# Optimization experiments

Measured on AMD Instinct MI355X. Metric: run time of the kernel, lower is better.

Reference implementation:

```python
import jax, jax.numpy as jnp
import numpy as np

D_MODEL = 1024
NUM_HEADS = 16
SEG = 512            # segment_size
DIL = 4              # dilation_rate
HEAD_DIM = D_MODEL // NUM_HEADS


def setup_inputs() -> dict:
    key = jax.random.key(0)
    ks = jax.random.split(key, 5)
    B, S = 4, 4096
    sc = D_MODEL ** -0.5  # keep projected activations O(1) so softmax is not saturated
    def w(k):
        return jax.random.normal(k, (D_MODEL, D_MODEL), jnp.float32) * sc
    z = jnp.zeros((D_MODEL,), jnp.float32)
    return {
        "x": jax.random.normal(ks[0], (B, S, D_MODEL), jnp.float32),
        "Wq": w(ks[1]), "bq": z,
        "Wk": w(ks[2]), "bk": z,
        "Wv": w(ks[3]), "bv": z,
        "Wo": w(ks[4]), "bo": z,
    }


def reference(x, Wq, bq, Wk, bk, Wv, bv, Wo, bo):
    B, S, D = x.shape
    H, hd, seg, r = NUM_HEADS, HEAD_DIM, SEG, DIL
    scaling = hd ** -0.5

    Q = x @ Wq + bq
    K = x @ Wk + bk
    V = x @ Wv + bv

    pad = (-S) % seg
    if pad:
        Q = jnp.pad(Q, ((0, 0), (0, pad), (0, 0)))
        K = jnp.pad(K, ((0, 0), (0, pad), (0, 0)))
        V = jnp.pad(V, ((0, 0), (0, pad), (0, 0)))
    n = (S + pad) // seg          # num_segments
    sd = seg // r                 # dilated positions per segment per head

    # [B, n, sd, r, H, hd]: position within segment = t*r + offset
    def split(t):
        return t.reshape(B, n, sd, r, H, hd)

    offs = jnp.arange(H) % r      # per-head dilation offset sj = j % r
    hidx = jnp.arange(H)
    # vectorized per-head dilated gather -> [B, n, sd, H, hd]
    Qs = split(Q)[:, :, :, offs, hidx, :]
    Ks = split(K)[:, :, :, offs, hidx, :]
    Vs = split(V)[:, :, :, offs, hidx, :]

    # diagonal q.k score per dilated position, softmax over the segment's dilated positions
    scores = jnp.einsum('bnshd,bnshd->bnsh', Qs, Ks) * scaling
    probs = jax.nn.softmax(scores, axis=2)
    attn = probs[..., None] * Vs  # [B, n, sd, H, hd]

    # scatter back to each head's dilated positions; other positions stay zero
    out = jnp.zeros((B, n, sd, r, H, hd), x.dtype)
    out = out.at[:, :, :, offs, hidx, :].set(attn)
    out = out.reshape(B, n * seg, D)[:, :S]
    return out @ Wo + bo
```

## Files before the change

### kernel.cpp

```cpp
#include <hip/hip_runtime.h>
#include <hip/hip_bf16.h>

typedef unsigned short u16;
typedef unsigned int u32;
typedef __attribute__((ext_vector_type(8))) __bf16 bf16x8;
typedef __attribute__((ext_vector_type(4))) float f32x4;

#define NB 4
#define SQ 4096
#define DM 1024
#define RPC 4096

__device__ __forceinline__ u16 f2b(float f) {
  u32 u = __builtin_bit_cast(u32, f);
  u32 r = u + 0x7fffu + ((u >> 16) & 1u);
  return (u16)(r >> 16);
}
__device__ __forceinline__ u32 cvt2(float lo, float hi) {
  u16 a = __builtin_bit_cast(u16, __float2bfloat16(lo));
  u16 b = __builtin_bit_cast(u16, __float2bfloat16(hi));
  return (u32)a | ((u32)b << 16);
}
__device__ __forceinline__ float dot2(u32 q, u32 k) {
  float ql = __builtin_bit_cast(float, q << 16);
  float qh = __builtin_bit_cast(float, q & 0xffff0000u);
  float kl = __builtin_bit_cast(float, k << 16);
  float kh = __builtin_bit_cast(float, k & 0xffff0000u);
  return ql * kl + qh * kh;
}
__device__ __forceinline__ u32 mul2(u32 v, float p) {
  float lo = __builtin_bit_cast(float, v << 16) * p;
  float hi = __builtin_bit_cast(float, v & 0xffff0000u) * p;
  return (u32)f2b(lo) | ((u32)f2b(hi) << 16);
}
__device__ __forceinline__ void gll16(const void* g, void* l) {
  __builtin_amdgcn_global_load_lds(
      (const __attribute__((address_space(1))) void*)g,
      (__attribute__((address_space(3))) void*)l, 16, 0, 0);
}

__global__ __launch_bounds__(256) void trans_qkv(const float* __restrict__ Wq,
                                                 const float* __restrict__ Wk,
                                                 const float* __restrict__ Wv,
                                                 u16* __restrict__ WTp) {
  __shared__ float T[64][65];
  const int k0 = blockIdx.x * 64, j0 = blockIdx.y * 64, c = blockIdx.z;
  const int msel = j0 >> 8;
  const float* W = (msel == 0) ? Wq : ((msel == 1) ? Wk : Wv);
  const int slot = (j0 & 255) >> 6;
  const int colbase = (c + 4 * slot) * 64;
  const int tid = threadIdx.x;
  const int rr = tid >> 6, cc = tid & 63;
#pragma unroll
  for (int it = 0; it < 16; ++it) {
    const int kk = rr + it * 4;
    T[kk][cc] = W[(size_t)(k0 + kk) * 1024 + colbase + cc];
  }
  __syncthreads();
  const int k64 = k0 >> 6;
  const int u = cc >> 3, e = cc & 7;
#pragma unroll
  for (int it = 0; it < 16; ++it) {
    const int jj = rr + it * 4;
    const int j = j0 + jj;
    const int n0 = j >> 8, nrow = j & 255;
    const int p = u ^ (nrow & 7);
    WTp[((size_t)((c * 3 + n0) * 16 + k64)) * 16384 + nrow * 64 + p * 8 + e] = f2b(T[cc][jj]);
  }
}

__global__ __launch_bounds__(256) void trans_wo(const float* __restrict__ Wo,
                                                u16* __restrict__ WoTp) {
  __shared__ float T[64][65];
  const int j0 = blockIdx.x * 64, e0 = blockIdx.y * 64, c = blockIdx.z;
  const int rowbase = c * 64 + (j0 >> 6) * 256;
  const int tid = threadIdx.x;
  const int rr = tid >> 6, cc = tid & 63;
#pragma unroll
  for (int it = 0; it < 16; ++it) {
    const int jj = rr + it * 4;
    T[jj][cc] = Wo[(size_t)(rowbase + jj) * 1024 + e0 + cc];
  }
  __syncthreads();
  const int k64 = j0 >> 6;
  const int u = cc >> 3, e = cc & 7;
#pragma unroll
  for (int it = 0; it < 16; ++it) {
    const int ee = rr + it * 4;
    const int n = e0 + ee;
    const int n0 = n >> 7, nrow = n & 127;
    const int p = u ^ (nrow & 7);
    WoTp[((size_t)((c * 8 + n0) * 4 + k64)) * 8192 + nrow * 64 + p * 8 + e] = f2b(T[cc][ee]);
  }
}

__global__ __launch_bounds__(256) void bias_pack(const float* __restrict__ bq,
                                                 const float* __restrict__ bk,
                                                 const float* __restrict__ bv,
                                                 float* __restrict__ biasp) {
  const int idx = blockIdx.x * 256 + threadIdx.x;
  if (idx >= 3072) return;
  const int c = idx / 768, j = idx % 768;
  const int msel = j >> 8, jj = j & 255;
  const int col = (c + 4 * (jj >> 6)) * 64 + (jj & 63);
  const float* bb = (msel == 0) ? bq : ((msel == 1) ? bk : bv);
  biasp[idx] = bb[col];
}

__global__ __launch_bounds__(256, 2) void gemm_qkv(const float* __restrict__ x,
                                                   const u16* __restrict__ WTp,
                                                   const float* __restrict__ biasp,
                                                   u16* __restrict__ QKV) {
  __shared__ __align__(16) u16 As[8192];
  __shared__ __align__(16) u16 Bs[16384];
  const int c = blockIdx.z, m0 = blockIdx.y, n0 = blockIdx.x;
  const int tid = threadIdx.x;
  const int lane = tid & 63, w = tid >> 6;
  const int wm = w >> 1, wn = w & 1;
  const int l15 = lane & 15, l16 = lane >> 4;

  f32x4 acc[4][8];
#pragma unroll
  for (int i = 0; i < 4; ++i)
#pragma unroll
    for (int j = 0; j < 8; ++j) acc[i][j] = (f32x4){0.f, 0.f, 0.f, 0.f};

  const int rbase = m0 * 128;
  const int b = rbase >> 10;
  const int sbase = ((rbase & 1023) << 2) + c;
  const float* xA = x + (size_t)(b * SQ + sbase) * DM;

  const int arow = tid >> 3, au = tid & 7;
  int awoff[4];
#pragma unroll
  for (int w4 = 0; w4 < 4; ++w4) {
    const int row = w4 * 32 + arow;
    awoff[w4] = row * 64 + ((au ^ (row & 7)) << 3);
  }
  const u16* Bsrc = WTp + (size_t)((c * 3 + n0) * 16) * 16384 + tid * 8;
  char* BsW = (char*)Bs + w * 1024;

  int aoff[2][4], boff[2][8];
#pragma unroll
  for (int kk = 0; kk < 2; ++kk) {
    const int unit = kk * 4 + l16;
#pragma unroll
    for (int mf = 0; mf < 4; ++mf) {
      const int row = wm * 64 + mf * 16 + l15;
      aoff[kk][mf] = row * 64 + ((unit ^ (row & 7)) << 3);
    }
#pragma unroll
    for (int nf = 0; nf < 8; ++nf) {
      const int row = wn * 128 + nf * 16 + l15;
      boff[kk][nf] = row * 64 + ((unit ^ (row & 7)) << 3);
    }
  }

  float4 av[8];
#pragma unroll
  for (int w4 = 0; w4 < 4; ++w4) {
    const float* s = xA + (size_t)(w4 * 32 + arow) * (4 * DM) + au * 8;
    av[2 * w4] = *reinterpret_cast<const float4*>(s);
    av[2 * w4 + 1] = *reinterpret_cast<const float4*>(s + 4);
  }

#pragma unroll 1
  for (int k64 = 0; k64 < 16; ++k64) {
    __syncthreads();
#pragma unroll
    for (int it = 0; it < 8; ++it)
      gll16(Bsrc + (size_t)k64 * 16384 + it * 2048, BsW + it * 4096);
#pragma unroll
    for (int w4 = 0; w4 < 4; ++w4) {
      uint4 pk;
      pk.x = cvt2(av[2 * w4].x, av[2 * w4].y);
      pk.y = cvt2(av[2 * w4].z, av[2 * w4].w);
      pk.z = cvt2(av[2 * w4 + 1].x, av[2 * w4 + 1].y);
      pk.w = cvt2(av[2 * w4 + 1].z, av[2 * w4 + 1].w);
      *reinterpret_cast<uint4*>(&As[awoff[w4]]) = pk;
    }
    __syncthreads();
    if (k64 < 15) {
      const int k0 = (k64 + 1) * 64;
#pragma unroll
      for (int w4 = 0; w4 < 4; ++w4) {
        const float* s = xA + (size_t)(w4 * 32 + arow) * (4 * DM) + k0 + au * 8;
        av[2 * w4] = *reinterpret_cast<const float4*>(s);
        av[2 * w4 + 1] = *reinterpret_cast<const float4*>(s + 4);
      }
    }
#pragma unroll
    for (int kk = 0; kk < 2; ++kk) {
      bf16x8 af[4], bv[8];
#pragma unroll
      for (int mf = 0; mf < 4; ++mf) af[mf] = *reinterpret_cast<const bf16x8*>(&As[aoff[kk][mf]]);
#pragma unroll
      for (int nf = 0; nf < 8; ++nf) bv[nf] = *reinterpret_cast<const bf16x8*>(&Bs[boff[kk][nf]]);
#pragma unroll
      for (int mf = 0; mf < 4; ++mf)
#pragma unroll
        for (int nf = 0; nf < 8; ++nf)
          acc[mf][nf] = __builtin_amdgcn_mfma_f32_16x16x32_bf16(af[mf], bv[nf], acc[mf][nf], 0, 0, 0);
    }
  }

  u16* outc = QKV + (size_t)c * RPC * 768;
#pragma unroll
  for (int mf = 0; mf < 4; ++mf) {
#pragma unroll
    for (int nf = 0; nf < 8; ++nf) {
      const int gcol = n0 * 256 + wn * 128 + nf * 16 + l15;
      const float bias = biasp[c * 768 + gcol];
#pragma unroll
      for (int jj = 0; jj < 4; ++jj) {
        const int rowt = wm * 64 + mf * 16 + l16 * 4 + jj;
        outc[(size_t)(rbase + rowt) * 768 + gcol] = f2b(acc[mf][nf][jj] + bias);
      }
    }
  }
}

__global__ __launch_bounds__(256) void attn_k(const u16* __restrict__ QKV,
                                              u16* __restrict__ attnYp) {
  __shared__ float sc[4][128];
  const int blk = blockIdx.x;
  const int c = blk >> 5, b = (blk >> 3) & 3, n = blk & 7;
  const int r0 = b * 1024 + n * 128;
  const int m0 = b * 8 + n;
  const u16* base = QKV + ((size_t)c * RPC + r0) * 768;
  const int tid = threadIdx.x;
#pragma unroll
  for (int it = 0; it < 2; ++it) {
    const int tt = tid + it * 256;
    const int t = tt & 127, slot = tt >> 7;
    const u16* q = base + (size_t)t * 768 + slot * 64;
    float s = 0.f;
#pragma unroll
    for (int dd = 0; dd < 8; ++dd) {
      uint4 qa = *reinterpret_cast<const uint4*>(q + dd * 8);
      uint4 ka = *reinterpret_cast<const uint4*>(q + 256 + dd * 8);
      s += dot2(qa.x, ka.x) + dot2(qa.y, ka.y) + dot2(qa.z, ka.z) + dot2(qa.w, ka.w);
    }
    sc[slot][t] = s * 0.125f;
  }
  __syncthreads();
  const int w = tid >> 6, lane = tid & 63;
  float v0 = sc[w][lane], v1 = sc[w][lane + 64];
  float m = fmaxf(v0, v1);
#pragma unroll
  for (int off = 32; off; off >>= 1) m = fmaxf(m, __shfl_xor(m, off));
  float e0 = __expf(v0 - m), e1 = __expf(v1 - m);
  float ssum = e0 + e1;
#pragma unroll
  for (int off = 32; off; off >>= 1) ssum += __shfl_xor(ssum, off);
  const float inv = 1.f / ssum;
  sc[w][lane] = e0 * inv;
  sc[w][lane + 64] = e1 * inv;
  __syncthreads();
  u16* yout = attnYp + (size_t)((c * 32 + m0) * 4) * 8192;
#pragma unroll
  for (int it = 0; it < 16; ++it) {
    const int vi = tid + it * 256;
    const int t = vi >> 5, c8 = vi & 31;
    const float p = sc[c8 >> 3][t];
    uint4 va = *reinterpret_cast<const uint4*>(base + (size_t)t * 768 + 512 + c8 * 8);
    uint4 ra;
    ra.x = mul2(va.x, p); ra.y = mul2(va.y, p); ra.z = mul2(va.z, p); ra.w = mul2(va.w, p);
    const int k64 = c8 >> 3, uu = c8 & 7, pp = uu ^ (t & 7);
    *reinterpret_cast<uint4*>(yout + k64 * 8192 + t * 64 + pp * 8) = ra;
  }
}

__global__ __launch_bounds__(256) void gemm_out(const u16* __restrict__ attnYp,
                                                const u16* __restrict__ WoTp,
                                                const float* __restrict__ bo,
                                                float* __restrict__ out) {
  __shared__ __align__(16) u16 As[8192];
  __shared__ __align__(16) u16 Bs[8192];
  const int c = blockIdx.z, m0 = blockIdx.y, n0 = blockIdx.x;
  const int tid = threadIdx.x;
  const int lane = tid & 63, w = tid >> 6;
  const int wm = w >> 1, wn = w & 1;
  const int l15 = lane & 15, l16 = lane >> 4;

  f32x4 acc[4][4];
#pragma unroll
  for (int i = 0; i < 4; ++i)
#pragma unroll
    for (int j = 0; j < 4; ++j) acc[i][j] = (f32x4){0.f, 0.f, 0.f, 0.f};

  const u16* Asrc = attnYp + (size_t)((c * 32 + m0) * 4) * 8192 + tid * 8;
  const u16* Bsrc = WoTp + (size_t)((c * 8 + n0) * 4) * 8192 + tid * 8;
  char* AsW = (char*)As + w * 1024;
  char* BsW = (char*)Bs + w * 1024;

  int aoff[2][4], boff[2][4];
#pragma unroll
  for (int kk = 0; kk < 2; ++kk) {
    const int unit = kk * 4 + l16;
#pragma unroll
    for (int f = 0; f < 4; ++f) {
      const int ra = wm * 64 + f * 16 + l15;
      aoff[kk][f] = ra * 64 + ((unit ^ (ra & 7)) << 3);
      const int rb = wn * 64 + f * 16 + l15;
      boff[kk][f] = rb * 64 + ((unit ^ (rb & 7)) << 3);
    }
  }

#pragma unroll 1
  for (int k64 = 0; k64 < 4; ++k64) {
    __syncthreads();
#pragma unroll
    for (int it = 0; it < 4; ++it) {
      gll16(Asrc + (size_t)k64 * 8192 + it * 2048, AsW + it * 4096);
      gll16(Bsrc + (size_t)k64 * 8192 + it * 2048, BsW + it * 4096);
    }
    __syncthreads();
#pragma unroll
    for (int kk = 0; kk < 2; ++kk) {
      bf16x8 af[4], bfv[4];
#pragma unroll
      for (int f = 0; f < 4; ++f) {
        af[f] = *reinterpret_cast<const bf16x8*>(&As[aoff[kk][f]]);
        bfv[f] = *reinterpret_cast<const bf16x8*>(&Bs[boff[kk][f]]);
      }
#pragma unroll
      for (int mf = 0; mf < 4; ++mf)
#pragma unroll
        for (int nf = 0; nf < 4; ++nf)
          acc[mf][nf] = __builtin_amdgcn_mfma_f32_16x16x32_bf16(af[mf], bfv[nf], acc[mf][nf], 0, 0, 0);
    }
  }

  const int rbase = m0 * 128;
  const int b = rbase >> 10;
  const int sbase = ((rbase & 1023) << 2) + c;
  float* outp = out + (size_t)(b * SQ + sbase) * DM;
#pragma unroll
  for (int mf = 0; mf < 4; ++mf) {
#pragma unroll
    for (int nf = 0; nf < 4; ++nf) {
      const int gcol = n0 * 128 + wn * 64 + nf * 16 + l15;
      const float bias = bo[gcol];
#pragma unroll
      for (int jj = 0; jj < 4; ++jj) {
        const int rowt = wm * 64 + mf * 16 + l16 * 4 + jj;
        outp[(size_t)rowt * (4 * DM) + gcol] = acc[mf][nf][jj] + bias;
      }
    }
  }
}

extern "C" void kernel_launch(void* const* d_in, const int* in_sizes, int n_in,
                              void* d_out, int out_size, void* d_ws, size_t ws_size,
                              hipStream_t stream) {
  const float* x  = (const float*)d_in[0];
  const float* Wq = (const float*)d_in[1];
  const float* bq = (const float*)d_in[2];
  const float* Wk = (const float*)d_in[3];
  const float* bk = (const float*)d_in[4];
  const float* Wv = (const float*)d_in[5];
  const float* bv = (const float*)d_in[6];
  const float* Wo = (const float*)d_in[7];
  const float* bo = (const float*)d_in[8];
  float* out = (float*)d_out;

  char* ws = (char*)d_ws;
  u16*   WTp   = (u16*)(ws);
  float* biasp = (float*)(ws + 6291456);
  u16*   WoTp  = (u16*)(ws + 6303744);
  u16*   QKV   = (u16*)(ws + 8400896);
  u16*   attnYp= (u16*)(ws + 33566720);

  trans_qkv<<<dim3(16, 12, 4), 256, 0, stream>>>(Wq, Wk, Wv, WTp);
  bias_pack<<<12, 256, 0, stream>>>(bq, bk, bv, biasp);
  trans_wo<<<dim3(4, 16, 4), 256, 0, stream>>>(Wo, WoTp);
  gemm_qkv<<<dim3(3, 32, 4), 256, 0, stream>>>(x, WTp, biasp, QKV);
  attn_k<<<128, 256, 0, stream>>>(QKV, attnYp);
  gemm_out<<<dim3(8, 32, 4), 256, 0, stream>>>(attnYp, WoTp, bo, out);
}
```

Baseline: 99.21 us.

## Double-buffer both GEMMs with 512-thread 256-row tiles and swizzled block order

Both GEMMs move to 512-thread blocks with 256-row tiles and double-buffered LDS. Explicit vmcnt/lgkmcnt waits and raw barriers let the next K-tile load overlap the MFMAs on the current one, and setprio raises MFMA priority. Weight packing is re-laid for the new tile widths (192 and 256 columns), and the grid is linearised with a remapped block index to change L2 locality. Attention now uses 256 blocks, each handling half the V columns. The hand-written waitcnt counts are fragile: a wrong count would cause a race, and the larger LDS footprint may reduce occupancy.

```diff
diff --git a/kernel.cpp b/kernel.cpp
--- a/kernel.cpp
+++ b/kernel.cpp
@@ -10,6 +10,11 @@
 #define SQ 4096
 #define DM 1024
 #define RPC 4096
+#define S4 (4 * DM)
+
+#define VMCNT(n) asm volatile("s_waitcnt vmcnt(" #n ")" ::: "memory")
+#define LGKM0()  asm volatile("s_waitcnt lgkmcnt(0)" ::: "memory")
+#define BARRIER() asm volatile("s_barrier" ::: "memory")
 
 __device__ __forceinline__ u16 f2b(float f) {
   u32 u = __builtin_bit_cast(u32, f);
@@ -63,9 +68,9 @@
   for (int it = 0; it < 16; ++it) {
     const int jj = rr + it * 4;
     const int j = j0 + jj;
-    const int n0 = j >> 8, nrow = j & 255;
-    const int p = u ^ (nrow & 7);
-    WTp[((size_t)((c * 3 + n0) * 16 + k64)) * 16384 + nrow * 64 + p * 8 + e] = f2b(T[cc][jj]);
+    const int n0 = j / 192, nrow = j - n0 * 192;
+    WTp[((size_t)((c * 4 + n0) * 16 + k64)) * 12288 + nrow * 64 + (((u ^ (nrow & 7))) << 3) + e] =
+        f2b(T[cc][jj]);
   }
 }
 
@@ -88,9 +93,9 @@
   for (int it = 0; it < 16; ++it) {
     const int ee = rr + it * 4;
     const int n = e0 + ee;
-    const int n0 = n >> 7, nrow = n & 127;
-    const int p = u ^ (nrow & 7);
-    WoTp[((size_t)((c * 8 + n0) * 4 + k64)) * 8192 + nrow * 64 + p * 8 + e] = f2b(T[cc][ee]);
+    const int n0 = n >> 8, nrow = n & 255;
+    WoTp[((size_t)((c * 4 + n0) * 4 + k64)) * 16384 + nrow * 64 + (((u ^ (nrow & 7))) << 3) + e] =
+        f2b(T[cc][ee]);
   }
 }
 
@@ -107,109 +112,138 @@
   biasp[idx] = bb[col];
 }
 
-__global__ __launch_bounds__(256, 2) void gemm_qkv(const float* __restrict__ x,
+__global__ __launch_bounds__(512, 2) void gemm_qkv(const float* __restrict__ x,
                                                    const u16* __restrict__ WTp,
                                                    const float* __restrict__ biasp,
                                                    u16* __restrict__ QKV) {
-  __shared__ __align__(16) u16 As[8192];
-  __shared__ __align__(16) u16 Bs[16384];
-  const int c = blockIdx.z, m0 = blockIdx.y, n0 = blockIdx.x;
+  __shared__ __align__(16) u16 As[2][16384];
+  __shared__ __align__(16) u16 Bs[2][12288];
+  const int p = blockIdx.x;
+  const int L = (p & 7) * 32 + (p >> 3);
+  const int c = L >> 6, rem = L & 63;
+  const int m0 = rem >> 2, n0 = rem & 3;
   const int tid = threadIdx.x;
   const int lane = tid & 63, w = tid >> 6;
   const int wm = w >> 1, wn = w & 1;
   const int l15 = lane & 15, l16 = lane >> 4;
 
-  f32x4 acc[4][8];
-#pragma unroll
-  for (int i = 0; i < 4; ++i)
-#pragma unroll
-    for (int j = 0; j < 8; ++j) acc[i][j] = (f32x4){0.f, 0.f, 0.f, 0.f};
-
-  const int rbase = m0 * 128;
+  const int rbase = m0 * 256;
   const int b = rbase >> 10;
   const int sbase = ((rbase & 1023) << 2) + c;
   const float* xA = x + (size_t)(b * SQ + sbase) * DM;
 
-  const int arow = tid >> 3, au = tid & 7;
   int awoff[4];
-#pragma unroll
-  for (int w4 = 0; w4 < 4; ++w4) {
-    const int row = w4 * 32 + arow;
-    awoff[w4] = row * 64 + ((au ^ (row & 7)) << 3);
-  }
-  const u16* Bsrc = WTp + (size_t)((c * 3 + n0) * 16) * 16384 + tid * 8;
-  char* BsW = (char*)Bs + w * 1024;
-
-  int aoff[2][4], boff[2][8];
+  const float* aptr[4];
+#pragma unroll
+  for (int j = 0; j < 4; ++j) {
+    const int r = (tid >> 3) + 64 * j;
+    awoff[j] = r * 64 + (((tid & 7) ^ (r & 7)) << 3);
+    aptr[j] = xA + (size_t)r * S4 + (tid & 7) * 8;
+  }
+  const u16* Bsrc = WTp + (size_t)((c * 4 + n0) * 16) * 12288;
+
+  f32x4 acc[4][6];
+#pragma unroll
+  for (int i = 0; i < 4; ++i)
+#pragma unroll
+    for (int j = 0; j < 6; ++j) acc[i][j] = (f32x4){0.f, 0.f, 0.f, 0.f};
+
+  int aoff[2][4], boff[2][6];
 #pragma unroll
   for (int kk = 0; kk < 2; ++kk) {
     const int unit = kk * 4 + l16;
 #pragma unroll
     for (int mf = 0; mf < 4; ++mf) {
-      const int row = wm * 64 + mf * 16 + l15;
-      aoff[kk][mf] = row * 64 + ((unit ^ (row & 7)) << 3);
-    }
-#pragma unroll
-    for (int nf = 0; nf < 8; ++nf) {
-      const int row = wn * 128 + nf * 16 + l15;
-      boff[kk][nf] = row * 64 + ((unit ^ (row & 7)) << 3);
+      const int r = wm * 64 + mf * 16 + l15;
+      aoff[kk][mf] = r * 64 + ((unit ^ (r & 7)) << 3);
+    }
+#pragma unroll
+    for (int nf = 0; nf < 6; ++nf) {
+      const int r = wn * 96 + nf * 16 + l15;
+      boff[kk][nf] = r * 64 + ((unit ^ (r & 7)) << 3);
     }
   }
 
   float4 av[8];
-#pragma unroll
-  for (int w4 = 0; w4 < 4; ++w4) {
-    const float* s = xA + (size_t)(w4 * 32 + arow) * (4 * DM) + au * 8;
-    av[2 * w4] = *reinterpret_cast<const float4*>(s);
-    av[2 * w4 + 1] = *reinterpret_cast<const float4*>(s + 4);
-  }
+
+#define LOADA(kt)                                                          \
+  {                                                                        \
+    _Pragma("unroll") for (int j = 0; j < 4; ++j) {                        \
+      const float* s = aptr[j] + (kt) * 64;                                \
+      av[2 * j] = *reinterpret_cast<const float4*>(s);                     \
+      av[2 * j + 1] = *reinterpret_cast<const float4*>(s + 4);             \
+    }                                                                      \
+  }
+#define DSWRITE(buf)                                                       \
+  {                                                                        \
+    _Pragma("unroll") for (int j = 0; j < 4; ++j) {                        \
+      uint4 pk;                                                            \
+      pk.x = cvt2(av[2 * j].x, av[2 * j].y);                               \
+      pk.y = cvt2(av[2 * j].z, av[2 * j].w);                               \
+      pk.z = cvt2(av[2 * j + 1].x, av[2 * j + 1].y);                       \
+      pk.w = cvt2(av[2 * j + 1].z, av[2 * j + 1].w);                       \
+      *reinterpret_cast<uint4*>(&As[buf][awoff[j]]) = pk;                  \
+    }                                                                      \
+  }
+#define ISSUE_B(kt, buf)                                                   \
+  {                                                                        \
+    _Pragma("unroll") for (int i = 0; i < 3; ++i)                          \
+        gll16(Bsrc + (size_t)(kt) * 12288 + tid * 8 + i * 4096,            \
+              (char*)&Bs[buf][0] + tid * 16 + i * 8192);                   \
+  }
+
+  LOADA(0);
+  DSWRITE(0);
+  LOADA(1);
+  ISSUE_B(0, 0);
+  ISSUE_B(1, 1);
+  VMCNT(6);
+  DSWRITE(1);
+  LOADA(2);
+  VMCNT(8);
+  LGKM0();
+  BARRIER();
 
 #pragma unroll 1
-  for (int k64 = 0; k64 < 16; ++k64) {
-    __syncthreads();
-#pragma unroll
-    for (int it = 0; it < 8; ++it)
-      gll16(Bsrc + (size_t)k64 * 16384 + it * 2048, BsW + it * 4096);
-#pragma unroll
-    for (int w4 = 0; w4 < 4; ++w4) {
-      uint4 pk;
-      pk.x = cvt2(av[2 * w4].x, av[2 * w4].y);
-      pk.y = cvt2(av[2 * w4].z, av[2 * w4].w);
-      pk.z = cvt2(av[2 * w4 + 1].x, av[2 * w4 + 1].y);
-      pk.w = cvt2(av[2 * w4 + 1].z, av[2 * w4 + 1].w);
-      *reinterpret_cast<uint4*>(&As[awoff[w4]]) = pk;
-    }
-    __syncthreads();
-    if (k64 < 15) {
-      const int k0 = (k64 + 1) * 64;
-#pragma unroll
-      for (int w4 = 0; w4 < 4; ++w4) {
-        const float* s = xA + (size_t)(w4 * 32 + arow) * (4 * DM) + k0 + au * 8;
-        av[2 * w4] = *reinterpret_cast<const float4*>(s);
-        av[2 * w4 + 1] = *reinterpret_cast<const float4*>(s + 4);
-      }
-    }
+  for (int t = 0; t < 16; ++t) {
+    const u16* Ab = As[t & 1];
+    const u16* Bb = Bs[t & 1];
 #pragma unroll
     for (int kk = 0; kk < 2; ++kk) {
-      bf16x8 af[4], bv[8];
-#pragma unroll
-      for (int mf = 0; mf < 4; ++mf) af[mf] = *reinterpret_cast<const bf16x8*>(&As[aoff[kk][mf]]);
-#pragma unroll
-      for (int nf = 0; nf < 8; ++nf) bv[nf] = *reinterpret_cast<const bf16x8*>(&Bs[boff[kk][nf]]);
+      bf16x8 af[4], bv[6];
+#pragma unroll
+      for (int mf = 0; mf < 4; ++mf) af[mf] = *reinterpret_cast<const bf16x8*>(Ab + aoff[kk][mf]);
+#pragma unroll
+      for (int nf = 0; nf < 6; ++nf) bv[nf] = *reinterpret_cast<const bf16x8*>(Bb + boff[kk][nf]);
+      __builtin_amdgcn_s_setprio(1);
 #pragma unroll
       for (int mf = 0; mf < 4; ++mf)
 #pragma unroll
-        for (int nf = 0; nf < 8; ++nf)
+        for (int nf = 0; nf < 6; ++nf)
           acc[mf][nf] = __builtin_amdgcn_mfma_f32_16x16x32_bf16(af[mf], bv[nf], acc[mf][nf], 0, 0, 0);
-    }
+      __builtin_amdgcn_s_setprio(0);
+    }
+    if (t == 15) break;
+    BARRIER();
+    if (t <= 13) {
+      VMCNT(8);
+      ISSUE_B(t + 2, t & 1);
+      VMCNT(3);
+      DSWRITE(t & 1);
+      if (t <= 12) LOADA(t + 3);
+    } else {
+      VMCNT(0);
+    }
+    LGKM0();
+    BARRIER();
   }
 
   u16* outc = QKV + (size_t)c * RPC * 768;
 #pragma unroll
   for (int mf = 0; mf < 4; ++mf) {
 #pragma unroll
-    for (int nf = 0; nf < 8; ++nf) {
-      const int gcol = n0 * 256 + wn * 128 + nf * 16 + l15;
+    for (int nf = 0; nf < 6; ++nf) {
+      const int gcol = n0 * 192 + wn * 96 + nf * 16 + l15;
       const float bias = biasp[c * 768 + gcol];
 #pragma unroll
       for (int jj = 0; jj < 4; ++jj) {
@@ -218,15 +252,19 @@
       }
     }
   }
+#undef LOADA
+#undef DSWRITE
+#undef ISSUE_B
 }
 
 __global__ __launch_bounds__(256) void attn_k(const u16* __restrict__ QKV,
                                               u16* __restrict__ attnYp) {
   __shared__ float sc[4][128];
   const int blk = blockIdx.x;
-  const int c = blk >> 5, b = (blk >> 3) & 3, n = blk & 7;
+  const int c = blk >> 6, b = (blk >> 4) & 3, n = (blk >> 1) & 7, half = blk & 1;
   const int r0 = b * 1024 + n * 128;
-  const int m0 = b * 8 + n;
+  const int m0 = r0 >> 8;
+  const int rb = r0 & 255;
   const u16* base = QKV + ((size_t)c * RPC + r0) * 768;
   const int tid = threadIdx.x;
 #pragma unroll
@@ -257,95 +295,121 @@
   sc[w][lane] = e0 * inv;
   sc[w][lane + 64] = e1 * inv;
   __syncthreads();
-  u16* yout = attnYp + (size_t)((c * 32 + m0) * 4) * 8192;
-#pragma unroll
-  for (int it = 0; it < 16; ++it) {
+  u16* yout = attnYp + (size_t)((c * 16 + m0) * 4) * 16384;
+#pragma unroll
+  for (int it = 0; it < 8; ++it) {
     const int vi = tid + it * 256;
-    const int t = vi >> 5, c8 = vi & 31;
-    const float p = sc[c8 >> 3][t];
+    const int t = vi >> 4, c8 = (vi & 15) + half * 16;
+    const float pr = sc[c8 >> 3][t];
     uint4 va = *reinterpret_cast<const uint4*>(base + (size_t)t * 768 + 512 + c8 * 8);
     uint4 ra;
-    ra.x = mul2(va.x, p); ra.y = mul2(va.y, p); ra.z = mul2(va.z, p); ra.w = mul2(va.w, p);
-    const int k64 = c8 >> 3, uu = c8 & 7, pp = uu ^ (t & 7);
-    *reinterpret_cast<uint4*>(yout + k64 * 8192 + t * 64 + pp * 8) = ra;
-  }
-}
-
-__global__ __launch_bounds__(256) void gemm_out(const u16* __restrict__ attnYp,
-                                                const u16* __restrict__ WoTp,
-                                                const float* __restrict__ bo,
-                                                float* __restrict__ out) {
-  __shared__ __align__(16) u16 As[8192];
-  __shared__ __align__(16) u16 Bs[8192];
-  const int c = blockIdx.z, m0 = blockIdx.y, n0 = blockIdx.x;
+    ra.x = mul2(va.x, pr); ra.y = mul2(va.y, pr); ra.z = mul2(va.z, pr); ra.w = mul2(va.w, pr);
+    const int rloc = rb + t;
+    const int k64 = c8 >> 3, uu = c8 & 7, pp = uu ^ (rloc & 7);
+    *reinterpret_cast<uint4*>(yout + k64 * 16384 + rloc * 64 + pp * 8) = ra;
+  }
+}
+
+__global__ __launch_bounds__(512, 2) void gemm_out(const u16* __restrict__ attnYp,
+                                                   const u16* __restrict__ WoTp,
+                                                   const float* __restrict__ bo,
+                                                   float* __restrict__ out) {
+  __shared__ __align__(16) u16 As[2][16384];
+  __shared__ __align__(16) u16 Bs[2][16384];
+  const int p = blockIdx.x;
+  const int L = (p & 7) * 32 + (p >> 3);
+  const int c = L >> 6, rem = L & 63;
+  const int m0 = rem >> 2, n0 = rem & 3;
   const int tid = threadIdx.x;
   const int lane = tid & 63, w = tid >> 6;
   const int wm = w >> 1, wn = w & 1;
   const int l15 = lane & 15, l16 = lane >> 4;
 
-  f32x4 acc[4][4];
+  const u16* Asrc = attnYp + (size_t)((c * 16 + m0) * 4) * 16384;
+  const u16* Bsrc = WoTp + (size_t)((c * 4 + n0) * 4) * 16384;
+
+  f32x4 acc[4][8];
 #pragma unroll
   for (int i = 0; i < 4; ++i)
 #pragma unroll
-    for (int j = 0; j < 4; ++j) acc[i][j] = (f32x4){0.f, 0.f, 0.f, 0.f};
-
-  const u16* Asrc = attnYp + (size_t)((c * 32 + m0) * 4) * 8192 + tid * 8;
-  const u16* Bsrc = WoTp + (size_t)((c * 8 + n0) * 4) * 8192 + tid * 8;
-  char* AsW = (char*)As + w * 1024;
-  char* BsW = (char*)Bs + w * 1024;
-
-  int aoff[2][4], boff[2][4];
+    for (int j = 0; j < 8; ++j) acc[i][j] = (f32x4){0.f, 0.f, 0.f, 0.f};
+
+  int aoff[2][4], boff[2][8];
 #pragma unroll
   for (int kk = 0; kk < 2; ++kk) {
     const int unit = kk * 4 + l16;
 #pragma unroll
-    for (int f = 0; f < 4; ++f) {
-      const int ra = wm * 64 + f * 16 + l15;
-      aoff[kk][f] = ra * 64 + ((unit ^ (ra & 7)) << 3);
-      const int rb = wn * 64 + f * 16 + l15;
-      boff[kk][f] = rb * 64 + ((unit ^ (rb & 7)) << 3);
-    }
-  }
+    for (int mf = 0; mf < 4; ++mf) {
+      const int r = wm * 64 + mf * 16 + l15;
+      aoff[kk][mf] = r * 64 + ((unit ^ (r & 7)) << 3);
+    }
+#pragma unroll
+    for (int nf = 0; nf < 8; ++nf) {
+      const int r = wn * 128 + nf * 16 + l15;
+      boff[kk][nf] = r * 64 + ((unit ^ (r & 7)) << 3);
+    }
+  }
+
+#define ISSUE(kt, buf)                                                     \
+  {                                                                        \
+    _Pragma("unroll") for (int i = 0; i < 4; ++i) {                        \
+      gll16(Asrc + (size_t)(kt) * 16384 + tid * 8 + i * 4096,              \
+            (char*)&As[buf][0] + tid * 16 + i * 8192);                     \
+      gll16(Bsrc + (size_t)(kt) * 16384 + tid * 8 + i * 4096,              \
+            (char*)&Bs[buf][0] + tid * 16 + i * 8192);                     \
+    }                                                                      \
+  }
+
+  ISSUE(0, 0);
+  ISSUE(1, 1);
+  VMCNT(8);
+  BARRIER();
 
 #pragma unroll 1
-  for (int k64 = 0; k64 < 4; ++k64) {
-    __syncthreads();
-#pragma unroll
-    for (int it = 0; it < 4; ++it) {
-      gll16(Asrc + (size_t)k64 * 8192 + it * 2048, AsW + it * 4096);
-      gll16(Bsrc + (size_t)k64 * 8192 + it * 2048, BsW + it * 4096);
-    }
-    __syncthreads();
+  for (int t = 0; t < 4; ++t) {
+    const u16* Ab = As[t & 1];
+    const u16* Bb = Bs[t & 1];
 #pragma unroll
     for (int kk = 0; kk < 2; ++kk) {
-      bf16x8 af[4], bfv[4];
-#pragma unroll
-      for (int f = 0; f < 4; ++f) {
-        af[f] = *reinterpret_cast<const bf16x8*>(&As[aoff[kk][f]]);
-        bfv[f] = *reinterpret_cast<const bf16x8*>(&Bs[boff[kk][f]]);
-      }
+      bf16x8 af[4], bv[8];
+#pragma unroll
+      for (int mf = 0; mf < 4; ++mf) af[mf] = *reinterpret_cast<const bf16x8*>(Ab + aoff[kk][mf]);
+#pragma unroll
+      for (int nf = 0; nf < 8; ++nf) bv[nf] = *reinterpret_cast<const bf16x8*>(Bb + boff[kk][nf]);
+      __builtin_amdgcn_s_setprio(1);
 #pragma unroll
       for (int mf = 0; mf < 4; ++mf)
 #pragma unroll
-        for (int nf = 0; nf < 4; ++nf)
-          acc[mf][nf] = __builtin_amdgcn_mfma_f32_16x16x32_bf16(af[mf], bfv[nf], acc[mf][nf], 0, 0, 0);
-    }
-  }
-
-  const int rbase = m0 * 128;
+        for (int nf = 0; nf < 8; ++nf)
+          acc[mf][nf] = __builtin_amdgcn_mfma_f32_16x16x32_bf16(af[mf], bv[nf], acc[mf][nf], 0, 0, 0);
+      __builtin_amdgcn_s_setprio(0);
+    }
+    if (t == 3) break;
+    BARRIER();
+    if (t <= 1) {
+      ISSUE(t + 2, t & 1);
+      VMCNT(8);
+    } else {
+      VMCNT(0);
+    }
+    BARRIER();
+  }
+#undef ISSUE
+
+  const int rbase = m0 * 256;
   const int b = rbase >> 10;
   const int sbase = ((rbase & 1023) << 2) + c;
   float* outp = out + (size_t)(b * SQ + sbase) * DM;
 #pragma unroll
   for (int mf = 0; mf < 4; ++mf) {
 #pragma unroll
-    for (int nf = 0; nf < 4; ++nf) {
-      const int gcol = n0 * 128 + wn * 64 + nf * 16 + l15;
+    for (int nf = 0; nf < 8; ++nf) {
+      const int gcol = n0 * 256 + wn * 128 + nf * 16 + l15;
       const float bias = bo[gcol];
 #pragma unroll
       for (int jj = 0; jj < 4; ++jj) {
         const int rowt = wm * 64 + mf * 16 + l16 * 4 + jj;
-        outp[(size_t)rowt * (4 * DM) + gcol] = acc[mf][nf][jj] + bias;
+        outp[(size_t)rowt * S4 + gcol] = acc[mf][nf][jj] + bias;
       }
     }
   }
@@ -375,7 +439,7 @@
   trans_qkv<<<dim3(16, 12, 4), 256, 0, stream>>>(Wq, Wk, Wv, WTp);
   bias_pack<<<12, 256, 0, stream>>>(bq, bk, bv, biasp);
   trans_wo<<<dim3(4, 16, 4), 256, 0, stream>>>(Wo, WoTp);
-  gemm_qkv<<<dim3(3, 32, 4), 256, 0, stream>>>(x, WTp, biasp, QKV);
-  attn_k<<<128, 256, 0, stream>>>(QKV, attnYp);
-  gemm_out<<<dim3(8, 32, 4), 256, 0, stream>>>(attnYp, WoTp, bo, out);
-}
+  gemm_qkv<<<256, 512, 0, stream>>>(x, WTp, biasp, QKV);
+  attn_k<<<256, 256, 0, stream>>>(QKV, attnYp);
+  gemm_out<<<256, 512, 0, stream>>>(attnYp, WoTp, bo, out);
+}
```

Result: faster. 84.05 us (-15.3%).
